# Kernel optimization log

Measured on AMD Instinct MI355X. Metric: run time of the kernel, lower is better.

The kernel has to match this reference:

```python
import jax, jax.numpy as jnp
import numpy as np
from jax import lax

BLANK = 0
LOGZERO = -1e30  # finite stand-in for -inf (keeps grads NaN-free, exact in fp32 logaddexp)


def setup_inputs() -> dict:
    key = jax.random.key(0)
    k1, k2 = jax.random.split(key)
    T, B, V, S = 512, 32, 4096, 128
    logits = jax.random.normal(k1, (T, B, V), dtype=jnp.float32)
    log_probs = jax.nn.log_softmax(logits, axis=-1)
    targets = jax.random.randint(k2, (B, S), 1, V, dtype=jnp.int32)  # avoid blank label
    input_lengths = jnp.full((B,), T, dtype=jnp.int32)   # must be >= 2*S+1
    target_lengths = jnp.full((B,), S, dtype=jnp.int32)
    return {"log_probs": log_probs, "targets": targets,
            "input_lengths": input_lengths, "target_lengths": target_lengths}


def _shift_right(a, n):
    # a: (B, L) log-space; shift states right by n, filling with log(0)
    pad = jnp.full(a.shape[:-1] + (n,), LOGZERO, dtype=a.dtype)
    return jnp.concatenate([pad, a[..., :-n]], axis=-1)


def _ctc_log_likelihood(log_probs, targets, input_lengths, target_lengths):
    # Vectorized CTC forward (alpha) recursion over the blank-interleaved trellis.
    # Mathematically identical to the per-sample bounded DP in the torch module:
    # states outside the reachability bounds carry log(0) / never feed the terminal sum.
    T, B, V = log_probs.shape
    S = targets.shape[1]
    L = 2 * S + 1
    blanked = jnp.full((B, L), BLANK, dtype=jnp.int32).at[:, 1::2].set(targets)
    # emission log-prob of each trellis state at each time: (T, B, L)
    emit = jnp.take_along_axis(log_probs, jnp.broadcast_to(blanked[None], (T, B, L)), axis=2)
    idx = jnp.arange(L)
    # skip transition (j-2 -> j) allowed for label states whose label differs from previous label
    skip = (idx % 2 == 1) & (idx >= 2) & (blanked != jnp.roll(blanked, 2, axis=1))  # (B, L)

    alpha0 = jnp.full((B, L), LOGZERO, dtype=log_probs.dtype)
    alpha0 = alpha0.at[:, 0].set(emit[0, :, 0]).at[:, 1].set(emit[0, :, 1])

    def step(alpha, xs):
        emit_t, t = xs  # emit_t: (B, L)
        pre = jnp.logaddexp(alpha, _shift_right(alpha, 1))
        pre = jnp.where(skip, jnp.logaddexp(pre, _shift_right(alpha, 2)), pre)
        new = emit_t + pre
        new = jnp.where((t < input_lengths)[:, None], new, alpha)  # freeze past each sample's length
        return new, None

    alpha, _ = lax.scan(step, alpha0, (emit[1:], jnp.arange(1, T)))
    b = jnp.arange(B)
    end = 2 * target_lengths  # final blank state index per sample
    ll = jnp.logaddexp(alpha[b, end], alpha[b, end - 1])  # log p(target | input)
    return ll


def reference(log_probs, targets, input_lengths, target_lengths):
    ll = _ctc_log_likelihood(log_probs, targets, input_lengths, target_lengths)
    B = log_probs.shape[1]
    # faithful to the module's 'mean' branch: (ret / target_lengths / B).sum()  (NOT negated)
    return (ll / target_lengths.astype(ll.dtype) / B).sum()
```

## Files before the change

kernel.cpp:

```cpp
#include <hip/hip_runtime.h>
#include <hip/hip_bf16.h>
#include <cstdint>

typedef unsigned short u16;
typedef uint32_t u32;

constexpr int Tc = 512, Bc = 32, Vc = 4096, Sc = 128;
constexpr int BOOST = 13;
constexpr int BSTRIDE = 576;
constexpr float LOG2E = 1.4426950408889634f;
constexpr float LN2 = 0.6931471805599453f;
constexpr int NT = 4;

__device__ __forceinline__ float bflo(u32 p) { return __uint_as_float(p << 16); }
__device__ __forceinline__ float bfhi(u32 p) { return __uint_as_float(p & 0xffff0000u); }

__device__ __forceinline__ u32 f2bf_bits(float f) {
    __hip_bfloat16 h = __float2bfloat16(f);
    return (u32)(*reinterpret_cast<u16*>(&h));
}

#define RLF(v, i) __int_as_float(__builtin_amdgcn_readlane(__float_as_int(v), (i)))

__global__ __launch_bounds__(256) void k_gather(const float* __restrict__ lp,
                                                const int* __restrict__ tgt,
                                                u32* __restrict__ emitT,
                                                float* __restrict__ blankT) {
    const int b = blockIdx.y;
    const int lane = threadIdx.x & 63;
    const int wv = threadIdx.x >> 6;
    const int t0 = (blockIdx.x * 4 + wv) * NT;

    const int tg0 = tgt[b * Sc + 2 * lane];
    const int tg1 = tgt[b * Sc + 2 * lane + 1];

    const float* row0 = lp + ((size_t)t0 * Bc + b) * Vc;
    float v0[NT], v1[NT], vb[NT];
#pragma unroll
    for (int i = 0; i < NT; ++i) {
        const float* row = row0 + (size_t)i * (Bc * Vc);
        v0[i] = row[tg0];
        v1[i] = row[tg1];
        vb[i] = row[0];
    }

    u32* orow = emitT + ((size_t)b * Tc + t0) * 64 + lane;
    float* bout = blankT + b * BSTRIDE + t0;
#pragma unroll
    for (int i = 0; i < NT; ++i) {
        const float e0 = __builtin_amdgcn_exp2f(fmaf(v0[i], LOG2E, (float)BOOST));
        const float e1 = __builtin_amdgcn_exp2f(fmaf(v1[i], LOG2E, (float)BOOST));
        orow[i * 64] = f2bf_bits(e0) | (f2bf_bits(e1) << 16);
        const float eb = __builtin_amdgcn_exp2f(fmaf(vb[i], LOG2E, (float)BOOST));
        if (lane == 0) bout[i] = eb;
    }
}

template <int CTRL, int RMASK>
__device__ __forceinline__ float dppmax(float v) {
    int t = __builtin_amdgcn_update_dpp(__float_as_int(v), __float_as_int(v),
                                        CTRL, RMASK, 0xf, false);
    return fmaxf(v, __int_as_float(t));
}
__device__ __forceinline__ float wave_max_bcast(float v) {
    v = dppmax<0x111, 0xf>(v);
    v = dppmax<0x112, 0xf>(v);
    v = dppmax<0x114, 0xf>(v);
    v = dppmax<0x118, 0xf>(v);
    v = dppmax<0x142, 0xa>(v);
    v = dppmax<0x143, 0xc>(v);
    return __int_as_float(__builtin_amdgcn_readlane(__float_as_int(v), 63));
}

__device__ __forceinline__ float wave_shr1(float v) {
    return __int_as_float(__builtin_amdgcn_update_dpp(
        0, __float_as_int(v), 0x138, 0xf, 0xf, true));
}

__global__ __launch_bounds__(64) void k_ctc(const u32* __restrict__ emitT,
                                            const float* __restrict__ blankT,
                                            const int* __restrict__ tgt,
                                            const int* __restrict__ in_len,
                                            const int* __restrict__ tg_len,
                                            float* __restrict__ out) {
    const int b = blockIdx.x;
    const int lane = threadIdx.x;
    const u32* p = emitT + (size_t)b * Tc * 64;
    const float* brow = blankT + b * BSTRIDE;

    const int tg0 = tgt[b * Sc + 2 * lane];
    const int tg1 = tgt[b * Sc + 2 * lane + 1];
    const int tgm = (lane > 0) ? tgt[b * Sc + 2 * lane - 1] : tg0;
    const float m1 = (lane > 0 && tg0 != tgm) ? 1.f : 0.f;
    const float m3 = (tg1 != tg0) ? 1.f : 0.f;
    const float sel = (lane == 63) ? 1.f : 0.f;

    const int steps = min(in_len[b], Tc) - 1;

    const u32 p0 = p[lane];
    float a0 = (lane == 0) ? brow[0] : 0.f;
    float a1 = (lane == 0) ? bflo(p0) : 0.f;
    float a2 = 0.f, a3 = 0.f, a4 = 0.f;
    int e_acc = 0;

    u32 pk[32];
    const u32* pr = p + 64;
#pragma unroll
    for (int d = 0; d < 32; ++d) pk[d] = pr[d * 64 + lane];
    const u32* pg = p + (size_t)33 * 64;

    float blkc = brow[1 + lane];

#define RENORM() {                                                  \
        float m = fmaxf(fmaxf(fmaxf(a0, a1), fmaxf(a2, a3)), a4);   \
        m = wave_max_bcast(m);                                      \
        int e = (int)((__float_as_uint(m) >> 23) & 0xffu) - 127;    \
        float scale = __uint_as_float((u32)(127 - e) << 23);        \
        a0 *= scale; a1 *= scale; a2 *= scale;                      \
        a3 *= scale; a4 *= scale;                                   \
        e_acc += e; }

#define GROUP_N(g) {                                                \
        const int H = ((g) & 1) * 16;                               \
        const int BI = (g) * 16;                                    \
        _Pragma("unroll")                                           \
        for (int d = 0; d < 16; ++d) {                              \
            const u32 pv = pk[H + d];                               \
            pk[H + d] = pg[d * 64 + lane];                          \
            const float ebl = RLF(blkc, BI + d);                    \
            const float e1 = bflo(pv);                              \
            const float e3 = bfhi(pv);                              \
            const float sh = wave_shr1(a3);                         \
            const float s01 = a0 + a1;                              \
            const float s12 = a1 + a2;                              \
            const float s23 = a2 + a3;                              \
            const float n0 = ebl * (a0 + sh);                       \
            const float n1 = e1 * fmaf(m1, sh, s01);                \
            const float n3 = e3 * fmaf(m3, a1, s23);                \
            a4 = ebl * fmaf(sel, a3, a4);                           \
            a0 = n0; a1 = n1; a2 = ebl * s12; a3 = n3;              \
            if (d == 7 || d == 15) RENORM()                         \
        }                                                           \
        pg += 16 * 64; }

#define GROUP_T(g) {                                                \
        const int H = ((g) & 1) * 16;                               \
        const int BI = (g) * 16;                                    \
        _Pragma("unroll")                                           \
        for (int d = 0; d < 16; ++d) {                              \
            const u32 pv = pk[H + d];                               \
            pk[H + d] = pg[d * 64 + lane];                          \
            const float ebl = RLF(blkc, BI + d);                    \
            const float e1 = bflo(pv);                              \
            const float e3 = bfhi(pv);                              \
            const float sh = wave_shr1(a3);                         \
            const float s01 = a0 + a1;                              \
            const float s12 = a1 + a2;                              \
            const float s23 = a2 + a3;                              \
            const float n0 = ebl * (a0 + sh);                       \
            const float n1 = e1 * fmaf(m1, sh, s01);                \
            const float n2 = ebl * s12;                             \
            const float n3 = e3 * fmaf(m3, a1, s23);                \
            const float n4 = ebl * fmaf(sel, a3, a4);               \
            const bool live = (t <= steps);                         \
            a0 = live ? n0 : a0; a1 = live ? n1 : a1;               \
            a2 = live ? n2 : a2; a3 = live ? n3 : a3;               \
            a4 = live ? n4 : a4;                                    \
            ++t;                                                    \
            if (d == 7 || d == 15) RENORM()                         \
        }                                                           \
        pg += 16 * 64; }

    const int nsb = steps >> 6;
    for (int sb = 0; sb < nsb; ++sb) {
        const float blkn = brow[(sb + 1) * 64 + 1 + lane];
        GROUP_N(0) GROUP_N(1) GROUP_N(2) GROUP_N(3)
        blkc = blkn;
    }
    int t = (nsb << 6) + 1;
    GROUP_T(0) GROUP_T(1) GROUP_T(2) GROUP_T(3)
#undef GROUP_N
#undef GROUP_T
#undef RENORM

    __shared__ float sa[257];
    sa[4 * lane + 0] = a0;
    sa[4 * lane + 1] = a1;
    sa[4 * lane + 2] = a2;
    sa[4 * lane + 3] = a3;
    if (lane == 63) sa[256] = a4;
    __syncthreads();
    if (lane == 0) {
        const int tl = tg_len[b];
        const int ei = 2 * tl;
        const float ssum = sa[ei] + sa[ei - 1];
        const float ll = __logf(ssum) +
                         LN2 * ((float)e_acc - (float)BOOST * (float)(steps + 1));
        atomicAdd(out, ll / (float)tl / (float)Bc);
    }
}

extern "C" void kernel_launch(void* const* d_in, const int* in_sizes, int n_in,
                              void* d_out, int out_size, void* d_ws, size_t ws_size,
                              hipStream_t stream) {
    const float* lp = (const float*)d_in[0];
    const int* tgt = (const int*)d_in[1];
    const int* in_len = (const int*)d_in[2];
    const int* tg_len = (const int*)d_in[3];

    char* ws = (char*)d_ws;
    float* blankT = (float*)ws;
    u32* emitT = (u32*)(ws + 128 * 1024);

    (void)hipMemsetAsync(d_out, 0, sizeof(float), stream);
    k_gather<<<dim3(Tc / (4 * NT), Bc), 256, 0, stream>>>(lp, tgt, emitT, blankT);
    k_ctc<<<Bc, 64, 0, stream>>>(emitT, blankT, tgt, in_len, tg_len, (float*)d_out);
}
```

Measured before the change: 365.0 us.

## Fuse gather and CTC recursion into one kernel with per-chunk readiness flags

Merges the emission-gather kernel and the serial CTC alpha recursion into a single launch. The first 32 blocks run the recursion and spin on per-batch, per-64-timestep atomic counters, while the remaining blocks gather and exponentiate emissions and signal completion with release atomics. This lets the serial recursion start before all emissions are gathered and removes one kernel boundary. It also replaces the shared-memory final reduction with readlane selects. It adds an extra memset, spin-wait polling, and a dependency on co-residency: if the gather blocks are not scheduled, the recursion blocks stall until a guard timeout.

```diff
diff --git a/kernel.cpp b/kernel.cpp
--- a/kernel.cpp
+++ b/kernel.cpp
@@ -10,7 +10,8 @@
 constexpr int BSTRIDE = 576;
 constexpr float LOG2E = 1.4426950408889634f;
 constexpr float LN2 = 0.6931471805599453f;
-constexpr int NT = 4;
+constexpr int NCHUNK = Tc / 64;
+constexpr int WAVES_PER_CHUNK = 16;
 
 __device__ __forceinline__ float bflo(u32 p) { return __uint_as_float(p << 16); }
 __device__ __forceinline__ float bfhi(u32 p) { return __uint_as_float(p & 0xffff0000u); }
@@ -21,40 +22,6 @@
 }
 
 #define RLF(v, i) __int_as_float(__builtin_amdgcn_readlane(__float_as_int(v), (i)))
-
-__global__ __launch_bounds__(256) void k_gather(const float* __restrict__ lp,
-                                                const int* __restrict__ tgt,
-                                                u32* __restrict__ emitT,
-                                                float* __restrict__ blankT) {
-    const int b = blockIdx.y;
-    const int lane = threadIdx.x & 63;
-    const int wv = threadIdx.x >> 6;
-    const int t0 = (blockIdx.x * 4 + wv) * NT;
-
-    const int tg0 = tgt[b * Sc + 2 * lane];
-    const int tg1 = tgt[b * Sc + 2 * lane + 1];
-
-    const float* row0 = lp + ((size_t)t0 * Bc + b) * Vc;
-    float v0[NT], v1[NT], vb[NT];
-#pragma unroll
-    for (int i = 0; i < NT; ++i) {
-        const float* row = row0 + (size_t)i * (Bc * Vc);
-        v0[i] = row[tg0];
-        v1[i] = row[tg1];
-        vb[i] = row[0];
-    }
-
-    u32* orow = emitT + ((size_t)b * Tc + t0) * 64 + lane;
-    float* bout = blankT + b * BSTRIDE + t0;
-#pragma unroll
-    for (int i = 0; i < NT; ++i) {
-        const float e0 = __builtin_amdgcn_exp2f(fmaf(v0[i], LOG2E, (float)BOOST));
-        const float e1 = __builtin_amdgcn_exp2f(fmaf(v1[i], LOG2E, (float)BOOST));
-        orow[i * 64] = f2bf_bits(e0) | (f2bf_bits(e1) << 16);
-        const float eb = __builtin_amdgcn_exp2f(fmaf(vb[i], LOG2E, (float)BOOST));
-        if (lane == 0) bout[i] = eb;
-    }
-}
 
 template <int CTRL, int RMASK>
 __device__ __forceinline__ float dppmax(float v) {
@@ -77,16 +44,68 @@
         0, __float_as_int(v), 0x138, 0xf, 0xf, true));
 }
 
-__global__ __launch_bounds__(64) void k_ctc(const u32* __restrict__ emitT,
-                                            const float* __restrict__ blankT,
-                                            const int* __restrict__ tgt,
-                                            const int* __restrict__ in_len,
-                                            const int* __restrict__ tg_len,
-                                            float* __restrict__ out) {
+__global__ __launch_bounds__(256) void k_fused(const float* __restrict__ lp,
+                                               const int* __restrict__ tgt,
+                                               u32* __restrict__ emitT,
+                                               float* __restrict__ blankT,
+                                               u32* cnt,
+                                               const int* __restrict__ in_len,
+                                               const int* __restrict__ tg_len,
+                                               float* __restrict__ out) {
+    if (blockIdx.x >= (unsigned)Bc) {
+        const int g = blockIdx.x - Bc;
+        const int b = g & (Bc - 1);
+        const int slab = g >> 5;
+        const int lane = threadIdx.x & 63;
+        const int wv = threadIdx.x >> 6;
+        const int t0 = slab * 16 + wv * 4;
+
+        const int tg0 = tgt[b * Sc + 2 * lane];
+        const int tg1 = tgt[b * Sc + 2 * lane + 1];
+
+        const float* row0 = lp + ((size_t)t0 * Bc + b) * Vc;
+        float v0[4], v1[4], vb[4];
+#pragma unroll
+        for (int i = 0; i < 4; ++i) {
+            const float* row = row0 + (size_t)i * (Bc * Vc);
+            v0[i] = row[tg0];
+            v1[i] = row[tg1];
+            vb[i] = row[0];
+        }
+
+        u32* orow = emitT + ((size_t)b * Tc + t0) * 64 + lane;
+        float* bout = blankT + b * BSTRIDE + t0;
+#pragma unroll
+        for (int i = 0; i < 4; ++i) {
+            const float e0 = __builtin_amdgcn_exp2f(fmaf(v0[i], LOG2E, (float)BOOST));
+            const float e1 = __builtin_amdgcn_exp2f(fmaf(v1[i], LOG2E, (float)BOOST));
+            orow[i * 64] = f2bf_bits(e0) | (f2bf_bits(e1) << 16);
+            const float eb = __builtin_amdgcn_exp2f(fmaf(vb[i], LOG2E, (float)BOOST));
+            if (lane == 0) bout[i] = eb;
+        }
+
+        __threadfence();
+        if (lane == 0)
+            __hip_atomic_fetch_add(&cnt[b * NCHUNK + (t0 >> 6)], 1u,
+                                   __ATOMIC_RELEASE, __HIP_MEMORY_SCOPE_AGENT);
+        return;
+    }
+
+    if (threadIdx.x >= 64) return;
     const int b = blockIdx.x;
     const int lane = threadIdx.x;
     const u32* p = emitT + (size_t)b * Tc * 64;
     const float* brow = blankT + b * BSTRIDE;
+    const u32* cb = cnt + b * NCHUNK;
+    int wlim = -1;
+
+#define WAITC(c) { int cc = (c); if (cc > NCHUNK - 1) cc = NCHUNK - 1;      \
+        while (wlim < cc) { ++wlim; u32 guard = 0;                           \
+            while (__hip_atomic_load(&cb[wlim], __ATOMIC_ACQUIRE,            \
+                                     __HIP_MEMORY_SCOPE_AGENT) <             \
+                   (u32)WAVES_PER_CHUNK) {                                   \
+                if (++guard > (1u << 26)) break;   \
+                __builtin_amdgcn_s_sleep(2); } } }
 
     const int tg0 = tgt[b * Sc + 2 * lane];
     const int tg1 = tgt[b * Sc + 2 * lane + 1];
@@ -96,6 +115,8 @@
     const float sel = (lane == 63) ? 1.f : 0.f;
 
     const int steps = min(in_len[b], Tc) - 1;
+
+    WAITC(1)
 
     const u32 p0 = p[lane];
     float a0 = (lane == 0) ? brow[0] : 0.f;
@@ -173,28 +194,35 @@
 
     const int nsb = steps >> 6;
     for (int sb = 0; sb < nsb; ++sb) {
+        WAITC(sb + 2)
         const float blkn = brow[(sb + 1) * 64 + 1 + lane];
         GROUP_N(0) GROUP_N(1) GROUP_N(2) GROUP_N(3)
         blkc = blkn;
     }
+    WAITC(nsb + 2)
     int t = (nsb << 6) + 1;
     GROUP_T(0) GROUP_T(1) GROUP_T(2) GROUP_T(3)
 #undef GROUP_N
 #undef GROUP_T
 #undef RENORM
-
-    __shared__ float sa[257];
-    sa[4 * lane + 0] = a0;
-    sa[4 * lane + 1] = a1;
-    sa[4 * lane + 2] = a2;
-    sa[4 * lane + 3] = a3;
-    if (lane == 63) sa[256] = a4;
-    __syncthreads();
+#undef WAITC
+
+    const int tl = tg_len[b];
+    const int ei = 2 * tl;
+    float vhi, vlo;
+    if (ei >= 256) {
+        vhi = RLF(a4, 63);
+        vlo = RLF(a3, 63);
+    } else {
+        const int r = ei & 3, l = ei >> 2;
+        const float x = (r == 0) ? a0 : (r == 1) ? a1 : (r == 2) ? a2 : a3;
+        vhi = RLF(x, l);
+        const int r2 = (ei - 1) & 3, l2 = (ei - 1) >> 2;
+        const float y = (r2 == 0) ? a0 : (r2 == 1) ? a1 : (r2 == 2) ? a2 : a3;
+        vlo = RLF(y, l2);
+    }
     if (lane == 0) {
-        const int tl = tg_len[b];
-        const int ei = 2 * tl;
-        const float ssum = sa[ei] + sa[ei - 1];
-        const float ll = __logf(ssum) +
+        const float ll = __logf(vhi + vlo) +
                          LN2 * ((float)e_acc - (float)BOOST * (float)(steps + 1));
         atomicAdd(out, ll / (float)tl / (float)Bc);
     }
@@ -210,9 +238,12 @@
 
     char* ws = (char*)d_ws;
     float* blankT = (float*)ws;
+    u32* cnt = (u32*)(ws + 96 * 1024);
     u32* emitT = (u32*)(ws + 128 * 1024);
 
     (void)hipMemsetAsync(d_out, 0, sizeof(float), stream);
-    k_gather<<<dim3(Tc / (4 * NT), Bc), 256, 0, stream>>>(lp, tgt, emitT, blankT);
-    k_ctc<<<Bc, 64, 0, stream>>>(emitT, blankT, tgt, in_len, tg_len, (float*)d_out);
-}
+    (void)hipMemsetAsync(cnt, 0, Bc * NCHUNK * sizeof(u32), stream);
+    const int grid = Bc + (Tc * Bc) / 16;
+    k_fused<<<grid, 256, 0, stream>>>(lp, tgt, emitT, blankT, cnt,
+                                      in_len, tg_len, (float*)d_out);
+}
```

Result: slower. 744.6 us (+104.0%).
